# Performance work log

Hardware: AMD Instinct MI355X
Metric: run time of the kernel (lower is better)

The kernel has to match this reference:

```python
import jax, jax.numpy as jnp
import numpy as np
import math


def proxy_delta_linear(x, W, gain):
    # x: [B,T,Din], W: [Dout,Din], gain: [1,1,Dout]
    D = x.shape[-1]
    xa = jnp.tanh(x)
    wa = jnp.tanh(W)
    x_sq = jnp.sum(xa * xa, axis=-1, keepdims=True)          # [B,T,1]
    w_sq = jnp.sum(wa * wa, axis=-1)                          # [Dout]
    dot = jnp.einsum('btd,od->bto', xa, wa)                   # [B,T,Dout]
    l2_sq = jnp.clip(x_sq + w_sq - 2.0 * dot, 0.0)
    out = 1.0 - l2_sq / D
    return (out - 0.5) * gain


def setup_inputs() -> dict:
    key = jax.random.key(0)
    ks = jax.random.split(key, 6)
    B, T, C = 2, 2048, 1024
    return {
        'x':  jax.random.normal(ks[0], (B, T, C), dtype=jnp.float32),
        'Wq': jax.random.normal(ks[1], (C, C), dtype=jnp.float32) * 0.02,
        'gq': jnp.full((1, 1, C), 2.0, dtype=jnp.float32),
        'Wk': jax.random.normal(ks[2], (C, C), dtype=jnp.float32) * 0.02,
        'gk': jnp.full((1, 1, C), 2.0, dtype=jnp.float32),
        'Wv': jax.random.normal(ks[3], (C, C), dtype=jnp.float32) * 0.02,
        'gv': jnp.full((1, 1, C), 2.0, dtype=jnp.float32),
        'Wo': jax.random.normal(ks[4], (C, C), dtype=jnp.float32) * 0.02,
    }


def reference(x, Wq, gq, Wk, gk, Wv, gv, Wo):
    B, T, C = x.shape
    H = 16
    D = C // H
    scale = math.sqrt(D)
    q = jnp.tanh(proxy_delta_linear(x, Wq, gq)).reshape(B, T, H, D).transpose(0, 2, 1, 3)
    k = jnp.tanh(proxy_delta_linear(x, Wk, gk)).reshape(B, T, H, D).transpose(0, 2, 1, 3)
    v = proxy_delta_linear(x, Wv, gv).reshape(B, T, H, D).transpose(0, 2, 1, 3)
    q_sq = jnp.sum(q * q, axis=-1, keepdims=True)             # [B,H,T,1]
    k_sq = jnp.sum(k * k, axis=-1)[:, :, None, :]             # [B,H,1,T]
    dot = jnp.einsum('bhtd,bhsd->bhts', q, k)                 # [B,H,T,T]
    dist_sq = jnp.clip(q_sq + k_sq - 2.0 * dot, 0.0)
    logits = -dist_sq / (scale * 10.0)
    attn = jax.nn.softmax(logits, axis=-1)
    out = jnp.einsum('bhts,bhsd->bhtd', attn, v)
    out = out.transpose(0, 2, 1, 3).reshape(B, T, C)
    return jnp.einsum('btc,oc->bto', out, Wo)
```

## Files before the change

kernel.cpp:

```cpp
#include <hip/hip_runtime.h>
#include <hip/hip_bf16.h>
#include <math.h>

typedef unsigned short u16;
typedef unsigned int u32;
typedef __attribute__((ext_vector_type(8))) short short8;
typedef __attribute__((ext_vector_type(8))) unsigned short ushort8;
typedef __attribute__((ext_vector_type(4))) float floatx4;
typedef __attribute__((ext_vector_type(16))) float floatx16;
typedef __attribute__((ext_vector_type(4))) u32 uint4v;
typedef __attribute__((ext_vector_type(2))) float float2v;
typedef __attribute__((ext_vector_type(2))) int int2v;

#define CDIM   1024
#define TSEQ   2048
#define NHEAD  16
#define HDIM   64

#define C2_CONST  (-0.01803368801111874f)
#define M2C2_CONST (0.03606737602223748f)

static __device__ __forceinline__ u16 f2bf(float f) {
    u32 u = __float_as_uint(f);
    u += 0x7fffu + ((u >> 16) & 1u);
    return (u16)(u >> 16);
}
static __device__ __forceinline__ float bf2f(u16 h) {
    return __uint_as_float(((u32)h) << 16);
}

static __device__ __forceinline__ u32 cvtpk(float a, float b) {
    u32 r;
    asm("v_cvt_pk_bf16_f32 %0, %1, %2" : "=v"(r) : "v"(a), "v"(b));
    return r;
}

static __device__ __forceinline__ float ftanh(float x) {
    float e = exp2f(x * 2.88539008f);
    float r = __builtin_amdgcn_rcpf(e + 1.0f);
    return fmaf(-2.0f, r, 1.0f);
}

static __device__ __forceinline__ void gll16(const void* g, void* l) {
    __builtin_amdgcn_global_load_lds(
        (const __attribute__((address_space(1))) unsigned int*)g,
        (__attribute__((address_space(3))) unsigned int*)l, 16, 0, 0);
}

__global__ __launch_bounds__(256) void prep(const float* __restrict__ x,
                                            const float* __restrict__ Wq, const float* __restrict__ Wk,
                                            const float* __restrict__ Wv, const float* __restrict__ Wo,
                                            u16* __restrict__ xa,
                                            u16* __restrict__ waq, u16* __restrict__ wak,
                                            u16* __restrict__ wav, u16* __restrict__ wob,
                                            float* __restrict__ xsq,
                                            float* __restrict__ sqq, float* __restrict__ sqk,
                                            float* __restrict__ sqv) {
    __shared__ float red[4];
    int bid = blockIdx.x, tid = threadIdx.x;
    const float* src; u16* dst; float* sq; int row; bool do_tanh = true;
    if (bid < 4096) {
        row = bid; src = x; dst = xa; sq = xsq;
    } else {
        int mat = (bid - 4096) >> 10; row = (bid - 4096) & 1023;
        src = (mat == 0) ? Wq : (mat == 1) ? Wk : (mat == 2) ? Wv : Wo;
        dst = (mat == 0) ? waq : (mat == 1) ? wak : (mat == 2) ? wav : wob;
        sq  = (mat == 0) ? sqq : (mat == 1) ? sqk : (mat == 2) ? sqv : nullptr;
        do_tanh = (mat < 3);
    }
    float4 v = reinterpret_cast<const float4*>(src + (size_t)row * CDIM)[tid];
    if (do_tanh) {
        float a0 = ftanh(v.x), a1 = ftanh(v.y), a2 = ftanh(v.z), a3 = ftanh(v.w);
        *reinterpret_cast<ushort4*>(dst + (size_t)row * CDIM + tid * 4) =
            make_ushort4(f2bf(a0), f2bf(a1), f2bf(a2), f2bf(a3));
        float s = a0*a0 + a1*a1 + a2*a2 + a3*a3;
        #pragma unroll
        for (int m = 1; m < 64; m <<= 1) s += __shfl_xor(s, m, 64);
        if ((tid & 63) == 0) red[tid >> 6] = s;
        __syncthreads();
        if (tid == 0 && sq) sq[row] = red[0] + red[1] + red[2] + red[3];
    } else {
        *reinterpret_cast<ushort4*>(dst + (size_t)row * CDIM + tid * 4) =
            make_ushort4(f2bf(v.x), f2bf(v.y), f2bf(v.z), f2bf(v.w));
    }
}

__global__ __launch_bounds__(256) void gemm_qkv(const u16* __restrict__ xa,
                                                const u16* __restrict__ waq, const u16* __restrict__ wak, const u16* __restrict__ wav,
                                                u16* __restrict__ qF, u16* __restrict__ kF, u16* __restrict__ vF,
                                                const float* __restrict__ xsq,
                                                const float* __restrict__ sqq, const float* __restrict__ sqk, const float* __restrict__ sqv,
                                                const float* __restrict__ gq, const float* __restrict__ gk, const float* __restrict__ gv) {
    __shared__ __align__(16) u16 As[128 * 64];
    __shared__ __align__(16) u16 Bs[128 * 64];
    int z = blockIdx.z;
    const u16* Bm     = (z == 0) ? waq : (z == 1) ? wak : wav;
    const float* wsq  = (z == 0) ? sqq : (z == 1) ? sqk : sqv;
    const float* gain = (z == 0) ? gq : (z == 1) ? gk : gv;

    int tid = threadIdx.x;
    int m0 = blockIdx.y * 128, n0 = blockIdx.x * 128;
    int w = tid >> 6, l = tid & 63, wm = w >> 1, wn = w & 1, g = l >> 4, c = l & 15;
    int r8 = l >> 3, sl7 = l & 7;
    int cmask = (c & 7) ^ (c >> 3);

    floatx4 acc[4][4] = {};

    for (int kt = 0; kt < 16; ++kt) {
        __syncthreads();
        #pragma unroll
        for (int i = 0; i < 4; i++) {
            int ch = w * 4 + i;
            int row = ch * 8 + r8;
            int sl = sl7 ^ r8 ^ (ch & 1);
            gll16(xa + (size_t)(m0 + row) * CDIM + kt * 64 + sl * 8, &As[ch * 512 + l * 8]);
            gll16(Bm + (size_t)(n0 + row) * CDIM + kt * 64 + sl * 8, &Bs[ch * 512 + l * 8]);
        }
        __syncthreads();
        short8 af[2][4], bf[2][4];
        #pragma unroll
        for (int kk = 0; kk < 2; kk++) {
            #pragma unroll
            for (int mi = 0; mi < 4; mi++)
                af[kk][mi] = *reinterpret_cast<const short8*>(
                    &As[(wm * 64 + mi * 16 + c) * 64 + (((kk * 4 + g) ^ cmask) << 3)]);
            #pragma unroll
            for (int ni = 0; ni < 4; ni++)
                bf[kk][ni] = *reinterpret_cast<const short8*>(
                    &Bs[(wn * 64 + ni * 16 + c) * 64 + (((kk * 4 + g) ^ cmask) << 3)]);
        }
        #pragma unroll
        for (int kk = 0; kk < 2; kk++)
            #pragma unroll
            for (int mi = 0; mi < 4; mi++)
                #pragma unroll
                for (int ni = 0; ni < 4; ni++)
                    acc[mi][ni] = __builtin_amdgcn_mfma_f32_16x16x32_bf16(af[kk][mi], bf[kk][ni], acc[mi][ni], 0, 0, 0);
    }

    if (z < 2) {
        u16* outF = (z == 0) ? qF : kF;
        #pragma unroll
        for (int mi = 0; mi < 4; mi++) {
            int rowb = m0 + wm * 64 + mi * 16 + g * 4;
            int bb = rowb >> 11, tt = rowb & 2047;
            int tile = tt >> 5, l31 = tt & 31;
            #pragma unroll
            for (int ni = 0; ni < 4; ni++) {
                int col = n0 + wn * 64 + ni * 16 + c;
                int hh = col >> 6, d = col & 63;
                int kst = d >> 4, hi8 = (d >> 3) & 1, j = d & 7;
                size_t base = ((((size_t)(bb * NHEAD + hh) * 64 + tile) * 4 + kst) * 2 + hi8) * 256 + j;
                float wsqc = wsq[col], gn = gain[col];
                #pragma unroll
                for (int r = 0; r < 4; r++) {
                    float l2 = fmaxf(xsq[rowb + r] + wsqc - 2.f * acc[mi][ni][r], 0.f);
                    float th = ftanh((0.5f - l2 * (1.f / 1024.f)) * gn);
                    outF[base + (size_t)(l31 + r) * 8] = f2bf(th);
                }
            }
        }
    } else {
        #pragma unroll
        for (int mi = 0; mi < 4; mi++) {
            int rowb = m0 + wm * 64 + mi * 16 + g * 4;
            int bb = rowb >> 11, s = rowb & 2047;
            int tile = s >> 5, e = (s >> 4) & 1, hi8 = (s >> 3) & 1, j0 = s & 7;
            #pragma unroll
            for (int ni = 0; ni < 4; ni++) {
                int col = n0 + wn * 64 + ni * 16 + c;
                int hh = col >> 6, d = col & 63;
                int dt = d >> 5, l31 = d & 31;
                float wsqc = wsq[col], gn = gain[col];
                float vals[4];
                #pragma unroll
                for (int r = 0; r < 4; r++) {
                    float l2 = fmaxf(xsq[rowb + r] + wsqc - 2.f * acc[mi][ni][r], 0.f);
                    vals[r] = (0.5f - l2 * (1.f / 1024.f)) * gn;
                }
                size_t idx = (((((size_t)(bb * NHEAD + hh) * 2 + dt) * 64 + tile) * 2 + e) * 2 + hi8) * 256
                             + (size_t)l31 * 8 + j0;
                *reinterpret_cast<ushort4*>(&vF[idx]) =
                    make_ushort4(f2bf(vals[0]), f2bf(vals[1]), f2bf(vals[2]), f2bf(vals[3]));
            }
        }
    }
}

__global__ __launch_bounds__(256) void knorm(const u16* __restrict__ kF,
                                             float* __restrict__ ksC2T) {
    int hb = blockIdx.x >> 3, seg = blockIdx.x & 7;
    int tile = seg * 8 + (threadIdx.x >> 5), t32 = threadIdx.x & 31;
    const u16* base = kF + ((size_t)hb * 64 + tile) * 2048 + t32 * 8;
    float s = 0.f;
    #pragma unroll
    for (int kst = 0; kst < 4; kst++)
        #pragma unroll
        for (int hi8 = 0; hi8 < 2; hi8++) {
            ushort8 v = *reinterpret_cast<const ushort8*>(base + (kst * 2 + hi8) * 256);
            #pragma unroll
            for (int j = 0; j < 8; j++) { float f = bf2f(v[j]); s += f * f; }
        }
    ksC2T[(size_t)hb * TSEQ + tile * 32 + t32] = s * C2_CONST;
}

__global__ __launch_bounds__(256) void gemm_out(const u16* __restrict__ A, const u16* __restrict__ Bm,
                                                float* __restrict__ outF) {
    __shared__ __align__(16) u16 As[128 * 64];
    __shared__ __align__(16) u16 Bs[128 * 64];
    int tid = threadIdx.x;
    int m0 = blockIdx.y * 128, n0 = blockIdx.x * 128;
    int w = tid >> 6, l = tid & 63, wm = w >> 1, wn = w & 1, g = l >> 4, c = l & 15;
    int r8 = l >> 3, sl7 = l & 7;
    int cmask = (c & 7) ^ (c >> 3);

    floatx4 acc[4][4] = {};

    for (int kt = 0; kt < 16; ++kt) {
        __syncthreads();
        #pragma unroll
        for (int i = 0; i < 4; i++) {
            int ch = w * 4 + i;
            int row = ch * 8 + r8;
            int sl = sl7 ^ r8 ^ (ch & 1);
            gll16(A + (size_t)(m0 + row) * CDIM + kt * 64 + sl * 8, &As[ch * 512 + l * 8]);
            gll16(Bm + (size_t)(n0 + row) * CDIM + kt * 64 + sl * 8, &Bs[ch * 512 + l * 8]);
        }
        __syncthreads();
        short8 af[2][4], bf[2][4];
        #pragma unroll
        for (int kk = 0; kk < 2; kk++) {
            #pragma unroll
            for (int mi = 0; mi < 4; mi++)
                af[kk][mi] = *reinterpret_cast<const short8*>(
                    &As[(wm * 64 + mi * 16 + c) * 64 + (((kk * 4 + g) ^ cmask) << 3)]);
            #pragma unroll
            for (int ni = 0; ni < 4; ni++)
                bf[kk][ni] = *reinterpret_cast<const short8*>(
                    &Bs[(wn * 64 + ni * 16 + c) * 64 + (((kk * 4 + g) ^ cmask) << 3)]);
        }
        #pragma unroll
        for (int kk = 0; kk < 2; kk++)
            #pragma unroll
            for (int mi = 0; mi < 4; mi++)
                #pragma unroll
                for (int ni = 0; ni < 4; ni++)
                    acc[mi][ni] = __builtin_amdgcn_mfma_f32_16x16x32_bf16(af[kk][mi], bf[kk][ni], acc[mi][ni], 0, 0, 0);
    }

    #pragma unroll
    for (int mi = 0; mi < 4; mi++) {
        int rowb = m0 + wm * 64 + mi * 16 + g * 4;
        #pragma unroll
        for (int ni = 0; ni < 4; ni++) {
            int col = n0 + wn * 64 + ni * 16 + c;
            #pragma unroll
            for (int r = 0; r < 4; r++)
                outF[(size_t)(rowb + r) * CDIM + col] = acc[mi][ni][r];
        }
    }
}

__global__ __launch_bounds__(256, 4) void attn10(const u16* __restrict__ qF, const u16* __restrict__ kF,
                                                 const u16* __restrict__ vF,
                                                 const float* __restrict__ ksC2T, u16* __restrict__ ao) {
    int bid = blockIdx.x;
    int hb = bid & 31;
    int ttile = bid >> 5;
    int tid = threadIdx.x, sc = tid >> 6, l = tid & 63;
    int hi = l >> 5, t32 = l & 31;

    __shared__ float redO[2][64][33];
    __shared__ float Ls[32];

    const u16* qbase = qF + ((size_t)hb * 64 + ttile) * 2048;
    short8 qf[4];
    #pragma unroll
    for (int ks = 0; ks < 4; ks++)
        qf[ks] = *reinterpret_cast<const short8*>(qbase + ks * 512 + (size_t)l * 8);

    const u16* kbase = kF + (size_t)hb * (64 * 2048);
    const u16* vbase = vF + (size_t)hb * (2 * 64 * 1024);
    const float* ksb = ksC2T + (size_t)hb * TSEQ;

    floatx16 oacc[2] = {};
    float2v l2a = {0.f, 0.f};
    const float2v m2v = {M2C2_CONST, M2C2_CONST};

    int st0 = sc * 16;
    #pragma unroll 2
    for (int st = st0; st < st0 + 16; ++st) {
        const short8* kp = reinterpret_cast<const short8*>(kbase + (size_t)st * 2048) + l;
        short8 kf0 = kp[0], kf1 = kp[64], kf2 = kp[128], kf3 = kp[192];
        const short8* vp = reinterpret_cast<const short8*>(vbase + (size_t)st * 1024) + l;
        short8 vf00 = vp[0], vf01 = vp[64];
        short8 vf10 = vp[8192], vf11 = vp[8256];

        __builtin_amdgcn_s_setprio(1);
        floatx16 sxx = {};
        sxx = __builtin_amdgcn_mfma_f32_32x32x16_bf16(kf0, qf[0], sxx, 0, 0, 0);
        sxx = __builtin_amdgcn_mfma_f32_32x32x16_bf16(kf1, qf[1], sxx, 0, 0, 0);
        sxx = __builtin_amdgcn_mfma_f32_32x32x16_bf16(kf2, qf[2], sxx, 0, 0, 0);
        sxx = __builtin_amdgcn_mfma_f32_32x32x16_bf16(kf3, qf[3], sxx, 0, 0, 0);
        __builtin_amdgcn_s_setprio(0);

        u32 pk[8];
        #pragma unroll
        for (int qq = 0; qq < 4; qq++) {
            float4 kc = *reinterpret_cast<const float4*>(&ksb[st * 32 + qq * 8 + hi * 4]);
            float2v s01 = {sxx[qq * 4 + 0], sxx[qq * 4 + 1]};
            float2v s23 = {sxx[qq * 4 + 2], sxx[qq * 4 + 3]};
            float2v a01 = s01 * m2v + (float2v){kc.x, kc.y};
            float2v a23 = s23 * m2v + (float2v){kc.z, kc.w};
            float p0 = exp2f(a01.x), p1 = exp2f(a01.y);
            float p2 = exp2f(a23.x), p3 = exp2f(a23.y);
            l2a += (float2v){p0, p1};
            l2a += (float2v){p2, p3};
            pk[qq * 2]     = cvtpk(p0, p1);
            pk[qq * 2 + 1] = cvtpk(p2, p3);
        }

        __builtin_amdgcn_s_setprio(1);
        #pragma unroll
        for (int e = 0; e < 2; e++) {
            int2v r02 = __builtin_amdgcn_permlane32_swap((int)pk[4 * e + 2], (int)pk[4 * e + 0], false, false);
            int2v r13 = __builtin_amdgcn_permlane32_swap((int)pk[4 * e + 3], (int)pk[4 * e + 1], false, false);
            uint4v au;
            au.x = (u32)r02.y;
            au.y = (u32)r13.y;
            au.z = (u32)r02.x;
            au.w = (u32)r13.x;
            short8 af = __builtin_bit_cast(short8, au);
            oacc[0] = __builtin_amdgcn_mfma_f32_32x32x16_bf16(af, e ? vf01 : vf00, oacc[0], 0, 0, 0);
            oacc[1] = __builtin_amdgcn_mfma_f32_32x32x16_bf16(af, e ? vf11 : vf10, oacc[1], 0, 0, 0);
        }
        __builtin_amdgcn_s_setprio(0);
    }
    float lrun = l2a.x + l2a.y;

    if (sc == 1 || sc == 3) {
        int sid = sc >> 1;
        #pragma unroll
        for (int dt = 0; dt < 2; dt++)
            #pragma unroll
            for (int r = 0; r < 16; r++)
                redO[sid][l][dt * 16 + r] = oacc[dt][r];
        redO[sid][l][32] = lrun;
    }
    __syncthreads();
    if (sc == 0 || sc == 2) {
        int sid = sc >> 1;
        #pragma unroll
        for (int dt = 0; dt < 2; dt++)
            #pragma unroll
            for (int r = 0; r < 16; r++)
                oacc[dt][r] += redO[sid][l][dt * 16 + r];
        lrun += redO[sid][l][32];
    }
    __syncthreads();
    if (sc == 2) {
        #pragma unroll
        for (int dt = 0; dt < 2; dt++)
            #pragma unroll
            for (int r = 0; r < 16; r++)
                redO[0][l][dt * 16 + r] = oacc[dt][r];
        redO[0][l][32] = lrun;
    }
    __syncthreads();
    if (sc == 0) {
        #pragma unroll
        for (int dt = 0; dt < 2; dt++)
            #pragma unroll
            for (int r = 0; r < 16; r++)
                oacc[dt][r] += redO[0][l][dt * 16 + r];
        lrun += redO[0][l][32];

        float ltot = lrun + __shfl_xor(lrun, 32, 64);
        if (l < 32) Ls[l] = ltot;
        int b = hb >> 4, h = hb & 15;
        int twb = ttile * 32;
        float4 lv[4];
        #pragma unroll
        for (int qq = 0; qq < 4; qq++)
            lv[qq] = *reinterpret_cast<const float4*>(&Ls[qq * 8 + hi * 4]);
        #pragma unroll
        for (int dt = 0; dt < 2; dt++)
            #pragma unroll
            for (int r = 0; r < 16; ++r) {
                int trow = (r & 3) + 8 * (r >> 2) + 4 * hi;
                float lval = (r & 3) == 0 ? lv[r >> 2].x : (r & 3) == 1 ? lv[r >> 2].y
                           : (r & 3) == 2 ? lv[r >> 2].z : lv[r >> 2].w;
                ao[(size_t)(b * TSEQ + twb + trow) * CDIM + h * HDIM + dt * 32 + t32] =
                    f2bf(oacc[dt][r] * __builtin_amdgcn_rcpf(lval));
            }
    }
}

extern "C" void kernel_launch(void* const* d_in, const int* in_sizes, int n_in,
                              void* d_out, int out_size, void* d_ws, size_t ws_size,
                              hipStream_t stream) {
    const float* x  = (const float*)d_in[0];
    const float* Wq = (const float*)d_in[1];
    const float* gq = (const float*)d_in[2];
    const float* Wk = (const float*)d_in[3];
    const float* gk = (const float*)d_in[4];
    const float* Wv = (const float*)d_in[5];
    const float* gv = (const float*)d_in[6];
    const float* Wo = (const float*)d_in[7];
    float* out = (float*)d_out;

    char* p = (char*)d_ws;
    u16* xa  = (u16*)p;  p += (size_t)8 << 20;
    u16* qF  = (u16*)p;  p += (size_t)8 << 20;
    u16* kF  = (u16*)p;  p += (size_t)8 << 20;
    u16* vF  = (u16*)p;  p += (size_t)8 << 20;
    u16* ao  = (u16*)p;  p += (size_t)8 << 20;
    u16* waq = (u16*)p;  p += (size_t)2 << 20;
    u16* wak = (u16*)p;  p += (size_t)2 << 20;
    u16* wav = (u16*)p;  p += (size_t)2 << 20;
    u16* wob = (u16*)p;  p += (size_t)2 << 20;
    float* xsq   = (float*)p; p += 4096 * 4;
    float* sqq   = (float*)p; p += 1024 * 4;
    float* sqk   = (float*)p; p += 1024 * 4;
    float* sqv   = (float*)p; p += 1024 * 4;
    float* ksC2T = (float*)p; p += 4096 * 16 * 4;
    (void)ws_size; (void)in_sizes; (void)n_in; (void)out_size;

    prep<<<8192, 256, 0, stream>>>(x, Wq, Wk, Wv, Wo, xa, waq, wak, wav, wob,
                                   xsq, sqq, sqk, sqv);

    dim3 gqkv(8, 32, 3);
    gemm_qkv<<<gqkv, 256, 0, stream>>>(xa, waq, wak, wav, qF, kF, vF, xsq,
                                       sqq, sqk, sqv, gq, gk, gv);

    knorm<<<256, 256, 0, stream>>>(kF, ksC2T);

    attn10<<<2048, 256, 0, stream>>>(qF, kF, vF, ksC2T, ao);

    dim3 gg(8, 32);
    gemm_out<<<gg, 256, 0, stream>>>(ao, wob, out);
}
```

Before: 143.0 us.

## Process two query tiles per attention block to reuse K/V loads

Each attention block now handles 64 query rows, as two 32-row sub-tiles, instead of 32, so every loaded K and V fragment feeds two score MFMAs and two PV MFMAs. The grid is halved and the launch-bounds occupancy hint drops from 4 to 2 to make room for the larger register set. The cross-wave reduction now runs twice with extra barriers, and the unroll pragma is removed. This cuts global K/V and key-norm traffic per unit of work, in exchange for higher register pressure and lower occupancy.

```diff
diff --git a/kernel.cpp b/kernel.cpp
--- a/kernel.cpp
+++ b/kernel.cpp
@@ -261,7 +261,7 @@
     }
 }
 
-__global__ __launch_bounds__(256, 4) void attn10(const u16* __restrict__ qF, const u16* __restrict__ kF,
+__global__ __launch_bounds__(256, 2) void attn11(const u16* __restrict__ qF, const u16* __restrict__ kF,
                                                  const u16* __restrict__ vF,
                                                  const float* __restrict__ ksC2T, u16* __restrict__ ao) {
     int bid = blockIdx.x;
@@ -273,22 +273,22 @@
     __shared__ float redO[2][64][33];
     __shared__ float Ls[32];
 
-    const u16* qbase = qF + ((size_t)hb * 64 + ttile) * 2048;
-    short8 qf[4];
+    const u16* qbase = qF + ((size_t)hb * 64 + ttile * 2) * 2048;
+    short8 qfA[4], qfB[4];
     #pragma unroll
-    for (int ks = 0; ks < 4; ks++)
-        qf[ks] = *reinterpret_cast<const short8*>(qbase + ks * 512 + (size_t)l * 8);
+    for (int ks = 0; ks < 4; ks++) {
+        qfA[ks] = *reinterpret_cast<const short8*>(qbase + ks * 512 + (size_t)l * 8);
+        qfB[ks] = *reinterpret_cast<const short8*>(qbase + 2048 + ks * 512 + (size_t)l * 8);
+    }
 
     const u16* kbase = kF + (size_t)hb * (64 * 2048);
     const u16* vbase = vF + (size_t)hb * (2 * 64 * 1024);
     const float* ksb = ksC2T + (size_t)hb * TSEQ;
 
-    floatx16 oacc[2] = {};
-    float2v l2a = {0.f, 0.f};
-    const float2v m2v = {M2C2_CONST, M2C2_CONST};
+    floatx16 oA[2] = {}, oB[2] = {};
+    float lA = 0.f, lB = 0.f;
 
     int st0 = sc * 16;
-    #pragma unroll 2
     for (int st = st0; st < st0 + 16; ++st) {
         const short8* kp = reinterpret_cast<const short8*>(kbase + (size_t)st * 2048) + l;
         short8 kf0 = kp[0], kf1 = kp[64], kf2 = kp[128], kf3 = kp[192];
@@ -296,103 +296,130 @@
         short8 vf00 = vp[0], vf01 = vp[64];
         short8 vf10 = vp[8192], vf11 = vp[8256];
 
+        float4 kc[4];
+        #pragma unroll
+        for (int qq = 0; qq < 4; qq++)
+            kc[qq] = *reinterpret_cast<const float4*>(&ksb[st * 32 + qq * 8 + hi * 4]);
+
         __builtin_amdgcn_s_setprio(1);
         floatx16 sxx = {};
-        sxx = __builtin_amdgcn_mfma_f32_32x32x16_bf16(kf0, qf[0], sxx, 0, 0, 0);
-        sxx = __builtin_amdgcn_mfma_f32_32x32x16_bf16(kf1, qf[1], sxx, 0, 0, 0);
-        sxx = __builtin_amdgcn_mfma_f32_32x32x16_bf16(kf2, qf[2], sxx, 0, 0, 0);
-        sxx = __builtin_amdgcn_mfma_f32_32x32x16_bf16(kf3, qf[3], sxx, 0, 0, 0);
+        sxx = __builtin_amdgcn_mfma_f32_32x32x16_bf16(kf0, qfA[0], sxx, 0, 0, 0);
+        sxx = __builtin_amdgcn_mfma_f32_32x32x16_bf16(kf1, qfA[1], sxx, 0, 0, 0);
+        sxx = __builtin_amdgcn_mfma_f32_32x32x16_bf16(kf2, qfA[2], sxx, 0, 0, 0);
+        sxx = __builtin_amdgcn_mfma_f32_32x32x16_bf16(kf3, qfA[3], sxx, 0, 0, 0);
         __builtin_amdgcn_s_setprio(0);
-
-        u32 pk[8];
+        u32 pkA[8];
         #pragma unroll
         for (int qq = 0; qq < 4; qq++) {
-            float4 kc = *reinterpret_cast<const float4*>(&ksb[st * 32 + qq * 8 + hi * 4]);
-            float2v s01 = {sxx[qq * 4 + 0], sxx[qq * 4 + 1]};
-            float2v s23 = {sxx[qq * 4 + 2], sxx[qq * 4 + 3]};
-            float2v a01 = s01 * m2v + (float2v){kc.x, kc.y};
-            float2v a23 = s23 * m2v + (float2v){kc.z, kc.w};
-            float p0 = exp2f(a01.x), p1 = exp2f(a01.y);
-            float p2 = exp2f(a23.x), p3 = exp2f(a23.y);
-            l2a += (float2v){p0, p1};
-            l2a += (float2v){p2, p3};
-            pk[qq * 2]     = cvtpk(p0, p1);
-            pk[qq * 2 + 1] = cvtpk(p2, p3);
+            float p0 = exp2f(fmaf(sxx[qq * 4 + 0], M2C2_CONST, kc[qq].x));
+            float p1 = exp2f(fmaf(sxx[qq * 4 + 1], M2C2_CONST, kc[qq].y));
+            float p2 = exp2f(fmaf(sxx[qq * 4 + 2], M2C2_CONST, kc[qq].z));
+            float p3 = exp2f(fmaf(sxx[qq * 4 + 3], M2C2_CONST, kc[qq].w));
+            lA += (p0 + p1) + (p2 + p3);
+            pkA[qq * 2]     = cvtpk(p0, p1);
+            pkA[qq * 2 + 1] = cvtpk(p2, p3);
         }
 
         __builtin_amdgcn_s_setprio(1);
+        floatx16 syy = {};
+        syy = __builtin_amdgcn_mfma_f32_32x32x16_bf16(kf0, qfB[0], syy, 0, 0, 0);
+        syy = __builtin_amdgcn_mfma_f32_32x32x16_bf16(kf1, qfB[1], syy, 0, 0, 0);
+        syy = __builtin_amdgcn_mfma_f32_32x32x16_bf16(kf2, qfB[2], syy, 0, 0, 0);
+        syy = __builtin_amdgcn_mfma_f32_32x32x16_bf16(kf3, qfB[3], syy, 0, 0, 0);
+        __builtin_amdgcn_s_setprio(0);
+        u32 pkB[8];
+        #pragma unroll
+        for (int qq = 0; qq < 4; qq++) {
+            float p0 = exp2f(fmaf(syy[qq * 4 + 0], M2C2_CONST, kc[qq].x));
+            float p1 = exp2f(fmaf(syy[qq * 4 + 1], M2C2_CONST, kc[qq].y));
+            float p2 = exp2f(fmaf(syy[qq * 4 + 2], M2C2_CONST, kc[qq].z));
+            float p3 = exp2f(fmaf(syy[qq * 4 + 3], M2C2_CONST, kc[qq].w));
+            lB += (p0 + p1) + (p2 + p3);
+            pkB[qq * 2]     = cvtpk(p0, p1);
+            pkB[qq * 2 + 1] = cvtpk(p2, p3);
+        }
+
+        __builtin_amdgcn_s_setprio(1);
         #pragma unroll
         for (int e = 0; e < 2; e++) {
-            int2v r02 = __builtin_amdgcn_permlane32_swap((int)pk[4 * e + 2], (int)pk[4 * e + 0], false, false);
-            int2v r13 = __builtin_amdgcn_permlane32_swap((int)pk[4 * e + 3], (int)pk[4 * e + 1], false, false);
-            uint4v au;
-            au.x = (u32)r02.y;
-            au.y = (u32)r13.y;
-            au.z = (u32)r02.x;
-            au.w = (u32)r13.x;
-            short8 af = __builtin_bit_cast(short8, au);
-            oacc[0] = __builtin_amdgcn_mfma_f32_32x32x16_bf16(af, e ? vf01 : vf00, oacc[0], 0, 0, 0);
-            oacc[1] = __builtin_amdgcn_mfma_f32_32x32x16_bf16(af, e ? vf11 : vf10, oacc[1], 0, 0, 0);
+            int2v a02 = __builtin_amdgcn_permlane32_swap((int)pkA[4 * e + 2], (int)pkA[4 * e + 0], false, false);
+            int2v a13 = __builtin_amdgcn_permlane32_swap((int)pkA[4 * e + 3], (int)pkA[4 * e + 1], false, false);
+            uint4v auA; auA.x = (u32)a02.y; auA.y = (u32)a13.y; auA.z = (u32)a02.x; auA.w = (u32)a13.x;
+            short8 afA = __builtin_bit_cast(short8, auA);
+            oA[0] = __builtin_amdgcn_mfma_f32_32x32x16_bf16(afA, e ? vf01 : vf00, oA[0], 0, 0, 0);
+            oA[1] = __builtin_amdgcn_mfma_f32_32x32x16_bf16(afA, e ? vf11 : vf10, oA[1], 0, 0, 0);
+
+            int2v b02 = __builtin_amdgcn_permlane32_swap((int)pkB[4 * e + 2], (int)pkB[4 * e + 0], false, false);
+            int2v b13 = __builtin_amdgcn_permlane32_swap((int)pkB[4 * e + 3], (int)pkB[4 * e + 1], false, false);
+            uint4v auB; auB.x = (u32)b02.y; auB.y = (u32)b13.y; auB.z = (u32)b02.x; auB.w = (u32)b13.x;
+            short8 afB = __builtin_bit_cast(short8, auB);
+            oB[0] = __builtin_amdgcn_mfma_f32_32x32x16_bf16(afB, e ? vf01 : vf00, oB[0], 0, 0, 0);
+            oB[1] = __builtin_amdgcn_mfma_f32_32x32x16_bf16(afB, e ? vf11 : vf10, oB[1], 0, 0, 0);
         }
         __builtin_amdgcn_s_setprio(0);
     }
-    float lrun = l2a.x + l2a.y;
-
-    if (sc == 1 || sc == 3) {
-        int sid = sc >> 1;
-        #pragma unroll
-        for (int dt = 0; dt < 2; dt++)
-            #pragma unroll
-            for (int r = 0; r < 16; r++)
-                redO[sid][l][dt * 16 + r] = oacc[dt][r];
-        redO[sid][l][32] = lrun;
-    }
-    __syncthreads();
-    if (sc == 0 || sc == 2) {
-        int sid = sc >> 1;
-        #pragma unroll
-        for (int dt = 0; dt < 2; dt++)
-            #pragma unroll
-            for (int r = 0; r < 16; r++)
-                oacc[dt][r] += redO[sid][l][dt * 16 + r];
-        lrun += redO[sid][l][32];
-    }
-    __syncthreads();
-    if (sc == 2) {
-        #pragma unroll
-        for (int dt = 0; dt < 2; dt++)
-            #pragma unroll
-            for (int r = 0; r < 16; r++)
-                redO[0][l][dt * 16 + r] = oacc[dt][r];
-        redO[0][l][32] = lrun;
-    }
-    __syncthreads();
-    if (sc == 0) {
-        #pragma unroll
-        for (int dt = 0; dt < 2; dt++)
-            #pragma unroll
-            for (int r = 0; r < 16; r++)
-                oacc[dt][r] += redO[0][l][dt * 16 + r];
-        lrun += redO[0][l][32];
-
-        float ltot = lrun + __shfl_xor(lrun, 32, 64);
-        if (l < 32) Ls[l] = ltot;
-        int b = hb >> 4, h = hb & 15;
-        int twb = ttile * 32;
-        float4 lv[4];
-        #pragma unroll
-        for (int qq = 0; qq < 4; qq++)
-            lv[qq] = *reinterpret_cast<const float4*>(&Ls[qq * 8 + hi * 4]);
-        #pragma unroll
-        for (int dt = 0; dt < 2; dt++)
-            #pragma unroll
-            for (int r = 0; r < 16; ++r) {
-                int trow = (r & 3) + 8 * (r >> 2) + 4 * hi;
-                float lval = (r & 3) == 0 ? lv[r >> 2].x : (r & 3) == 1 ? lv[r >> 2].y
-                           : (r & 3) == 2 ? lv[r >> 2].z : lv[r >> 2].w;
-                ao[(size_t)(b * TSEQ + twb + trow) * CDIM + h * HDIM + dt * 32 + t32] =
-                    f2bf(oacc[dt][r] * __builtin_amdgcn_rcpf(lval));
-            }
+
+    int b = hb >> 4, h = hb & 15;
+    #pragma unroll
+    for (int qs = 0; qs < 2; qs++) {
+        floatx16* oacc = qs ? oB : oA;
+        float lrun = qs ? lB : lA;
+        if (qs) __syncthreads();
+        if (sc == 1 || sc == 3) {
+            int sid = sc >> 1;
+            #pragma unroll
+            for (int dt = 0; dt < 2; dt++)
+                #pragma unroll
+                for (int r = 0; r < 16; r++)
+                    redO[sid][l][dt * 16 + r] = oacc[dt][r];
+            redO[sid][l][32] = lrun;
+        }
+        __syncthreads();
+        if (sc == 0 || sc == 2) {
+            int sid = sc >> 1;
+            #pragma unroll
+            for (int dt = 0; dt < 2; dt++)
+                #pragma unroll
+                for (int r = 0; r < 16; r++)
+                    oacc[dt][r] += redO[sid][l][dt * 16 + r];
+            lrun += redO[sid][l][32];
+        }
+        __syncthreads();
+        if (sc == 2) {
+            #pragma unroll
+            for (int dt = 0; dt < 2; dt++)
+                #pragma unroll
+                for (int r = 0; r < 16; r++)
+                    redO[0][l][dt * 16 + r] = oacc[dt][r];
+            redO[0][l][32] = lrun;
+        }
+        __syncthreads();
+        if (sc == 0) {
+            #pragma unroll
+            for (int dt = 0; dt < 2; dt++)
+                #pragma unroll
+                for (int r = 0; r < 16; r++)
+                    oacc[dt][r] += redO[0][l][dt * 16 + r];
+            lrun += redO[0][l][32];
+
+            float ltot = lrun + __shfl_xor(lrun, 32, 64);
+            if (l < 32) Ls[l] = ltot;
+            int twb = ttile * 64 + qs * 32;
+            float4 lv[4];
+            #pragma unroll
+            for (int qq = 0; qq < 4; qq++)
+                lv[qq] = *reinterpret_cast<const float4*>(&Ls[qq * 8 + hi * 4]);
+            #pragma unroll
+            for (int dt = 0; dt < 2; dt++)
+                #pragma unroll
+                for (int r = 0; r < 16; ++r) {
+                    int trow = (r & 3) + 8 * (r >> 2) + 4 * hi;
+                    float lval = (r & 3) == 0 ? lv[r >> 2].x : (r & 3) == 1 ? lv[r >> 2].y
+                               : (r & 3) == 2 ? lv[r >> 2].z : lv[r >> 2].w;
+                    ao[(size_t)(b * TSEQ + twb + trow) * CDIM + h * HDIM + dt * 32 + t32] =
+                        f2bf(oacc[dt][r] * __builtin_amdgcn_rcpf(lval));
+                }
+        }
     }
 }
 
@@ -435,7 +462,7 @@
 
     knorm<<<256, 256, 0, stream>>>(kF, ksC2T);
 
-    attn10<<<2048, 256, 0, stream>>>(qF, kF, vF, ksC2T, ao);
+    attn11<<<1024, 256, 0, stream>>>(qF, kF, vF, ksC2T, ao);
 
     dim3 gg(8, 32);
     gemm_out<<<gg, 256, 0, stream>>>(ao, wob, out);
```

After: 143.5 us. About the same (+0.3%).

## Stage QKV epilogue through shared memory for coalesced writes; scalarize softmax exp math

Applied to the files above, without the earlier changes.

The QKV GEMM epilogue now writes its tiled bf16 outputs into the reused shared-memory buffer first, then copies them to global memory as contiguous 16-byte vectors per head tile. This replaces scattered 2-byte and 8-byte global stores. The attention kernel's packed float2 FMA and accumulate are replaced by scalar fmaf with a single scalar running sum. The change adds extra barriers and LDS traffic, and relies on each block's 128 columns mapping to exactly two heads.

```diff
diff --git a/kernel.cpp b/kernel.cpp
--- a/kernel.cpp
+++ b/kernel.cpp
@@ -9,7 +9,6 @@
 typedef __attribute__((ext_vector_type(4))) float floatx4;
 typedef __attribute__((ext_vector_type(16))) float floatx16;
 typedef __attribute__((ext_vector_type(4))) u32 uint4v;
-typedef __attribute__((ext_vector_type(2))) float float2v;
 typedef __attribute__((ext_vector_type(2))) int int2v;
 
 #define CDIM   1024
@@ -91,8 +90,9 @@
                                                 const float* __restrict__ xsq,
                                                 const float* __restrict__ sqq, const float* __restrict__ sqk, const float* __restrict__ sqv,
                                                 const float* __restrict__ gq, const float* __restrict__ gk, const float* __restrict__ gv) {
-    __shared__ __align__(16) u16 As[128 * 64];
-    __shared__ __align__(16) u16 Bs[128 * 64];
+    __shared__ __align__(16) u16 SMEM[2 * 128 * 64];
+    u16* As = SMEM;
+    u16* Bs = SMEM + 128 * 64;
     int z = blockIdx.z;
     const u16* Bm     = (z == 0) ? waq : (z == 1) ? wak : wav;
     const float* wsq  = (z == 0) ? sqq : (z == 1) ? sqk : sqv;
@@ -138,38 +138,57 @@
                     acc[mi][ni] = __builtin_amdgcn_mfma_f32_16x16x32_bf16(af[kk][mi], bf[kk][ni], acc[mi][ni], 0, 0, 0);
     }
 
+    __syncthreads();
+
+    int bb = m0 >> 11;
+    int tile0 = (m0 & 2047) >> 5;
+    int hh0 = blockIdx.x * 2;
+
     if (z < 2) {
         u16* outF = (z == 0) ? qF : kF;
         #pragma unroll
         for (int mi = 0; mi < 4; mi++) {
             int rowb = m0 + wm * 64 + mi * 16 + g * 4;
-            int bb = rowb >> 11, tt = rowb & 2047;
-            int tile = tt >> 5, l31 = tt & 31;
+            int tile4 = (rowb & 127) >> 5;
+            int l31 = rowb & 31;
             #pragma unroll
             for (int ni = 0; ni < 4; ni++) {
                 int col = n0 + wn * 64 + ni * 16 + c;
-                int hh = col >> 6, d = col & 63;
+                int hh2 = (col >> 6) & 1;
+                int d = col & 63;
                 int kst = d >> 4, hi8 = (d >> 3) & 1, j = d & 7;
-                size_t base = ((((size_t)(bb * NHEAD + hh) * 64 + tile) * 4 + kst) * 2 + hi8) * 256 + j;
+                int lidx = hh2 * 8192 + tile4 * 2048 + kst * 512 + hi8 * 256 + l31 * 8 + j;
                 float wsqc = wsq[col], gn = gain[col];
                 #pragma unroll
                 for (int r = 0; r < 4; r++) {
                     float l2 = fmaxf(xsq[rowb + r] + wsqc - 2.f * acc[mi][ni][r], 0.f);
                     float th = ftanh((0.5f - l2 * (1.f / 1024.f)) * gn);
-                    outF[base + (size_t)(l31 + r) * 8] = f2bf(th);
+                    SMEM[lidx + r * 8] = f2bf(th);
                 }
             }
         }
+        __syncthreads();
+        #pragma unroll
+        for (int hh2 = 0; hh2 < 2; hh2++) {
+            u16* gdst = outF + (((size_t)(bb * NHEAD + hh0 + hh2) * 64 + tile0) * 2048);
+            #pragma unroll
+            for (int i = 0; i < 4; i++) {
+                int off = i * 2048 + tid * 8;
+                *reinterpret_cast<ushort8*>(gdst + off) =
+                    *reinterpret_cast<const ushort8*>(&SMEM[hh2 * 8192 + off]);
+            }
+        }
     } else {
         #pragma unroll
         for (int mi = 0; mi < 4; mi++) {
             int rowb = m0 + wm * 64 + mi * 16 + g * 4;
-            int bb = rowb >> 11, s = rowb & 2047;
-            int tile = s >> 5, e = (s >> 4) & 1, hi8 = (s >> 3) & 1, j0 = s & 7;
+            int tile4 = (rowb & 127) >> 5;
+            int e = (rowb >> 4) & 1, hi8 = (rowb >> 3) & 1, j0 = rowb & 7;
             #pragma unroll
             for (int ni = 0; ni < 4; ni++) {
                 int col = n0 + wn * 64 + ni * 16 + c;
-                int hh = col >> 6, d = col & 63;
+                int hh2 = (col >> 6) & 1;
+                int d = col & 63;
                 int dt = d >> 5, l31 = d & 31;
                 float wsqc = wsq[col], gn = gain[col];
                 float vals[4];
@@ -178,12 +197,24 @@
                     float l2 = fmaxf(xsq[rowb + r] + wsqc - 2.f * acc[mi][ni][r], 0.f);
                     vals[r] = (0.5f - l2 * (1.f / 1024.f)) * gn;
                 }
-                size_t idx = (((((size_t)(bb * NHEAD + hh) * 2 + dt) * 64 + tile) * 2 + e) * 2 + hi8) * 256
-                             + (size_t)l31 * 8 + j0;
-                *reinterpret_cast<ushort4*>(&vF[idx]) =
+                int lidx = hh2 * 8192 + dt * 4096 + tile4 * 1024 + e * 512 + hi8 * 256 + l31 * 8 + j0;
+                *reinterpret_cast<ushort4*>(&SMEM[lidx]) =
                     make_ushort4(f2bf(vals[0]), f2bf(vals[1]), f2bf(vals[2]), f2bf(vals[3]));
             }
         }
+        __syncthreads();
+        #pragma unroll
+        for (int hh2 = 0; hh2 < 2; hh2++)
+            #pragma unroll
+            for (int dt = 0; dt < 2; dt++) {
+                u16* gdst = vF + ((((size_t)(bb * NHEAD + hh0 + hh2) * 2 + dt) * 64 + tile0) * 1024);
+                #pragma unroll
+                for (int i = 0; i < 2; i++) {
+                    int off = i * 2048 + tid * 8;
+                    *reinterpret_cast<ushort8*>(gdst + off) =
+                        *reinterpret_cast<const ushort8*>(&SMEM[hh2 * 8192 + dt * 4096 + off]);
+                }
+            }
     }
 }
 
@@ -261,9 +292,9 @@
     }
 }
 
-__global__ __launch_bounds__(256, 4) void attn10(const u16* __restrict__ qF, const u16* __restrict__ kF,
-                                                 const u16* __restrict__ vF,
-                                                 const float* __restrict__ ksC2T, u16* __restrict__ ao) {
+__global__ __launch_bounds__(256, 4) void attn(const u16* __restrict__ qF, const u16* __restrict__ kF,
+                                               const u16* __restrict__ vF,
+                                               const float* __restrict__ ksC2T, u16* __restrict__ ao) {
     int bid = blockIdx.x;
     int hb = bid & 31;
     int ttile = bid >> 5;
@@ -284,8 +315,7 @@
     const float* ksb = ksC2T + (size_t)hb * TSEQ;
 
     floatx16 oacc[2] = {};
-    float2v l2a = {0.f, 0.f};
-    const float2v m2v = {M2C2_CONST, M2C2_CONST};
+    float lrun = 0.f;
 
     int st0 = sc * 16;
     #pragma unroll 2
@@ -308,14 +338,11 @@
         #pragma unroll
         for (int qq = 0; qq < 4; qq++) {
             float4 kc = *reinterpret_cast<const float4*>(&ksb[st * 32 + qq * 8 + hi * 4]);
-            float2v s01 = {sxx[qq * 4 + 0], sxx[qq * 4 + 1]};
-            float2v s23 = {sxx[qq * 4 + 2], sxx[qq * 4 + 3]};
-            float2v a01 = s01 * m2v + (float2v){kc.x, kc.y};
-            float2v a23 = s23 * m2v + (float2v){kc.z, kc.w};
-            float p0 = exp2f(a01.x), p1 = exp2f(a01.y);
-            float p2 = exp2f(a23.x), p3 = exp2f(a23.y);
-            l2a += (float2v){p0, p1};
-            l2a += (float2v){p2, p3};
+            float p0 = exp2f(fmaf(sxx[qq * 4 + 0], M2C2_CONST, kc.x));
+            float p1 = exp2f(fmaf(sxx[qq * 4 + 1], M2C2_CONST, kc.y));
+            float p2 = exp2f(fmaf(sxx[qq * 4 + 2], M2C2_CONST, kc.z));
+            float p3 = exp2f(fmaf(sxx[qq * 4 + 3], M2C2_CONST, kc.w));
+            lrun += (p0 + p1) + (p2 + p3);
             pk[qq * 2]     = cvtpk(p0, p1);
             pk[qq * 2 + 1] = cvtpk(p2, p3);
         }
@@ -336,7 +363,6 @@
         }
         __builtin_amdgcn_s_setprio(0);
     }
-    float lrun = l2a.x + l2a.y;
 
     if (sc == 1 || sc == 3) {
         int sid = sc >> 1;
@@ -435,7 +461,7 @@
 
     knorm<<<256, 256, 0, stream>>>(kF, ksC2T);
 
-    attn10<<<2048, 256, 0, stream>>>(qF, kF, vF, ksC2T, ao);
+    attn<<<2048, 256, 0, stream>>>(qF, kF, vF, ksC2T, ao);
 
     dim3 gg(8, 32);
     gemm_out<<<gg, 256, 0, stream>>>(ao, wob, out);
```

Result: no change. 143.2 us (+0.1%).
